# Performance work log

Measured on AMD Instinct MI355X. Metric: run time of the kernel, lower is better.

## Reference

```python
import jax, jax.numpy as jnp
import numpy as np

N_NODES, D, B, NEG2, DRUG_NUM = 20000, 512, 2048, 64, 2000
H1, H2 = 128, 64


def setup_inputs() -> dict:
    ks = jax.random.split(jax.random.key(0), 10)
    embed = jax.random.normal(ks[0], (N_NODES, D), dtype=jnp.float32)
    h = jax.random.randint(ks[1], (B, 1), 0, DRUG_NUM)
    t = jax.random.randint(ks[2], (B, 1), 0, N_NODES)
    n_s = jax.random.randint(ks[3], (B, NEG2), 0, DRUG_NUM)  # all < drug_num -> chunk branch
    s1 = 1.0 / np.sqrt(2 * D)
    s2 = 1.0 / np.sqrt(H1)
    s3 = 1.0 / np.sqrt(H2)
    W1 = jax.random.uniform(ks[4], (2 * D, H1), minval=-s1, maxval=s1, dtype=jnp.float32)
    b1 = jax.random.uniform(ks[5], (H1,), minval=-s1, maxval=s1, dtype=jnp.float32)
    W2 = jax.random.uniform(ks[6], (H1, H2), minval=-s2, maxval=s2, dtype=jnp.float32)
    b2 = jax.random.uniform(ks[7], (H2,), minval=-s2, maxval=s2, dtype=jnp.float32)
    W3 = jax.random.uniform(ks[8], (H2, 1), minval=-s3, maxval=s3, dtype=jnp.float32)
    b3 = jax.random.uniform(ks[9], (1,), minval=-s3, maxval=s3, dtype=jnp.float32)
    return {"embed": embed, "W1": W1, "b1": b1, "W2": W2, "b2": b2, "W3": W3, "b3": b3,
            "h": h, "t": t, "n_s": n_s}


def _mlp(x, W1, b1, W2, b2, W3, b3):
    # [..., 2D] -> [...] score
    x = jax.nn.relu(x @ W1 + b1)
    x = jax.nn.relu(x @ W2 + b2)
    return (x @ W3 + b3)[..., 0]


def reference(embed, W1, b1, W2, b2, W3, b3, h, t, n_s):
    K = n_s.shape[1] // 2
    n_t, n_h = n_s[:, :K], n_s[:, K:]
    h_e = embed[h]          # [B, 1, D]
    t_e = embed[t]          # [B, T, D]
    T = t.shape[1]
    # positive pairs: [B, T]
    pos = _mlp(jnp.concatenate([jnp.tile(h_e, (1, T, 1)), t_e], axis=-1),
               W1, b1, W2, b2, W3, b3)
    # corrupted-tail negatives: [B, K]
    neg1 = _mlp(jnp.concatenate([jnp.tile(h_e, (1, K, 1)), embed[n_t]], axis=-1),
                W1, b1, W2, b2, W3, b3)
    # corrupted-head negatives: [B, T*K] (T=1 here)
    neg2 = _mlp(jnp.concatenate([embed[n_h], jnp.tile(t_e, (1, K, 1))], axis=-1),
                W1, b1, W2, b2, W3, b3)
    neg = jnp.concatenate([neg1, neg2], axis=1)  # [B, 2K]
    return pos, neg
```

## Files before the change

### kernel.cpp

```cpp
#include <hip/hip_runtime.h>

#define DIM    512
#define BATCH  2048
#define NDRUG  2000
#define H1     128
#define H2     64
#define NITEM  65
#define SLAB   774144
#define W2F_OFF (4 * SLAB)
#define W1F_OFF (W2F_OFF + 4096)
#define X1_OFF  (W1F_OFF + 65536)
#define X2_OFF  (X1_OFF + 512000)

typedef __attribute__((ext_vector_type(8))) short short8;
typedef __attribute__((ext_vector_type(4))) float floatx4;

__device__ inline unsigned short f2bf(float x) {
    union { float f; unsigned u; } v; v.f = x;
    unsigned r = v.u + 0x7fffu + ((v.u >> 16) & 1u);
    return (unsigned short)(r >> 16);
}

__device__ inline short8 cvt8(const float* __restrict__ src) {
    float4 a = *(const float4*)src, b = *(const float4*)(src + 4);
    short8 v;
    v[0] = (short)f2bf(a.x); v[1] = (short)f2bf(a.y);
    v[2] = (short)f2bf(a.z); v[3] = (short)f2bf(a.w);
    v[4] = (short)f2bf(b.x); v[5] = (short)f2bf(b.y);
    v[6] = (short)f2bf(b.z); v[7] = (short)f2bf(b.w);
    return v;
}

__global__ __launch_bounds__(256) void prep(
    const float* __restrict__ embed, const float* __restrict__ W1,
    const float* __restrict__ W2, const int* __restrict__ t,
    float* __restrict__ ws)
{
    const int blk = blockIdx.x, tid = threadIdx.x;
    if (blk < 125) {
        short8* X1 = (short8*)(ws + X1_OFF);
        #pragma unroll
        for (int i = 0; i < 4; ++i) {
            int u = blk * 1024 + i * 256 + tid;
            int row = u >> 6, c = u & 63;
            X1[u] = cvt8(embed + (size_t)row * DIM + c * 8);
        }
    } else if (blk < 253) {
        short8* X2 = (short8*)(ws + X2_OFF);
        #pragma unroll
        for (int i = 0; i < 4; ++i) {
            int u = (blk - 125) * 1024 + i * 256 + tid;
            int row = u >> 6, c = u & 63;
            X2[u] = cvt8(embed + (size_t)t[row] * DIM + c * 8);
        }
    } else if (blk < 255) {
        short8* W1f = (short8*)(ws + W1F_OFF);
        #pragma unroll
        for (int i = 0; i < 32; ++i) {
            int item = (blk - 253) * 8192 + i * 256 + tid;
            int frag = item >> 6, lane = item & 63;
            int half = frag >> 7, ktot = (frag >> 3) & 15, nt = frag & 7;
            int n = lane & 15, q = lane >> 4;
            short8 v;
            #pragma unroll
            for (int j = 0; j < 8; ++j) {
                int k = half * DIM + ktot * 32 + q * 8 + j;
                v[j] = (short)f2bf(W1[k * H1 + nt * 16 + n]);
            }
            W1f[item] = v;
        }
    } else {
        short8* W2f = (short8*)(ws + W2F_OFF);
        #pragma unroll
        for (int i = 0; i < 4; ++i) {
            int item = i * 256 + tid;
            int frag = item >> 6, lane = item & 63;
            int kt = frag >> 2, nt = frag & 3;
            int n = lane & 15, q = lane >> 4;
            short8 v;
            #pragma unroll
            for (int j = 0; j < 8; ++j)
                v[j] = (short)f2bf(W2[(kt * 32 + q * 8 + j) * H2 + nt * 16 + n]);
            W2f[item] = v;
        }
    }
}

__global__ __launch_bounds__(256) void layer1_mfma(float* __restrict__ ws)
{
    const short8* W1f = (const short8*)(ws + W1F_OFF);
    const int lane = threadIdx.x & 63;
    const int w    = blockIdx.x * 4 + (threadIdx.x >> 6);
    const int n = lane & 15, q = lane >> 4;

    const short8* Xrow;
    float* obase;
    int half, ntsel, kc;
    if (w < 2000) {
        int rt = w >> 4, rem = w & 15, cg = rem >> 2;
        kc = rem & 3;
        Xrow = (const short8*)(ws + X1_OFF) + (size_t)(rt * 16 + n) * 64 + kc * 16;
        half  = cg >> 1;
        ntsel = (cg & 1) * 4;
        obase = ws + (size_t)kc * SLAB + half * (NDRUG * H1)
                   + (size_t)(rt * 16) * H1 + (cg & 1) * 64;
    } else {
        int w2 = w - 2000;
        int rt = w2 >> 3, rem = w2 & 7, cg = rem >> 2;
        kc = rem & 3;
        Xrow = (const short8*)(ws + X2_OFF) + (size_t)(rt * 16 + n) * 64 + kc * 16;
        half  = 1;
        ntsel = cg * 4;
        obase = ws + (size_t)kc * SLAB + 2 * (NDRUG * H1)
                   + (size_t)(rt * 16) * H1 + cg * 64;
    }

    floatx4 acc[4];
    #pragma unroll
    for (int nt = 0; nt < 4; ++nt) acc[nt] = (floatx4){0.f, 0.f, 0.f, 0.f};

    #pragma unroll
    for (int kt = 0; kt < 4; ++kt) {
        short8 af = Xrow[kt * 4 + q];
        #pragma unroll
        for (int nt = 0; nt < 4; ++nt) {
            short8 bf = W1f[(size_t)((half * 16 + kc * 4 + kt) * 8 + ntsel + nt) * 64 + lane];
            acc[nt] = __builtin_amdgcn_mfma_f32_16x16x32_bf16(af, bf, acc[nt], 0, 0, 0);
        }
    }

    #pragma unroll
    for (int nt = 0; nt < 4; ++nt)
        #pragma unroll
        for (int reg = 0; reg < 4; ++reg)
            obase[(q * 4 + reg) * H1 + nt * 16 + n] = acc[nt][reg];
}

__global__ __launch_bounds__(256) void reduce4(float* __restrict__ ws)
{
    int i = (blockIdx.x * 256 + threadIdx.x) * 8;
    #pragma unroll
    for (int half = 0; half < 2; ++half) {
        int o = i + half * 4;
        float4 a = *(const float4*)(ws + o);
        float4 b = *(const float4*)(ws + SLAB + o);
        float4 c = *(const float4*)(ws + 2 * SLAB + o);
        float4 d = *(const float4*)(ws + 3 * SLAB + o);
        a.x += b.x + c.x + d.x;  a.y += b.y + c.y + d.y;
        a.z += b.z + c.z + d.z;  a.w += b.w + c.w + d.w;
        *(float4*)(ws + o) = a;
    }
}

__global__ __launch_bounds__(256) void score_mfma(
    const float* __restrict__ ws,
    const float* __restrict__ b1, const float* __restrict__ b2,
    const float* __restrict__ W3, const float* __restrict__ b3,
    const int* __restrict__ h, const int* __restrict__ ns,
    float* __restrict__ out)
{
    const float* P  = ws;
    const float* Q  = ws + NDRUG * H1;
    const float* Qt = Q + NDRUG * H1;
    const short8* W2f = (const short8*)(ws + W2F_OFF);

    const int lane = threadIdx.x & 63;
    const int wv   = threadIdx.x >> 6;
    const int tile = blockIdx.x * 4 + wv;
    const int n = lane & 15, q = lane >> 4;

    const int sg   = tile * 16 + n;
    const int b    = sg / NITEM;
    const int item = sg - b * NITEM;
    const float *Pr, *Qr;
    if (item == 0)       { Pr = P + h[b] * H1;                        Qr = Qt + b * H1; }
    else if (item <= 32) { Pr = P + h[b] * H1;                        Qr = Q + ns[b * 64 + item - 1] * H1; }
    else                 { Pr = P + ns[b * 64 + 32 + item - 33] * H1; Qr = Qt + b * H1; }

    floatx4 acc[4];
    #pragma unroll
    for (int nt = 0; nt < 4; ++nt) acc[nt] = (floatx4){0.f, 0.f, 0.f, 0.f};

    #pragma unroll
    for (int kt = 0; kt < 4; ++kt) {
        const int kb = kt * 32 + q * 8;
        float4 p0 = *(const float4*)(Pr + kb);
        float4 p1 = *(const float4*)(Pr + kb + 4);
        float4 q0 = *(const float4*)(Qr + kb);
        float4 q1 = *(const float4*)(Qr + kb + 4);
        float4 c0 = *(const float4*)(b1 + kb);
        float4 c1 = *(const float4*)(b1 + kb + 4);
        short8 af;
        af[0] = (short)f2bf(fmaxf(p0.x + q0.x + c0.x, 0.f));
        af[1] = (short)f2bf(fmaxf(p0.y + q0.y + c0.y, 0.f));
        af[2] = (short)f2bf(fmaxf(p0.z + q0.z + c0.z, 0.f));
        af[3] = (short)f2bf(fmaxf(p0.w + q0.w + c0.w, 0.f));
        af[4] = (short)f2bf(fmaxf(p1.x + q1.x + c1.x, 0.f));
        af[5] = (short)f2bf(fmaxf(p1.y + q1.y + c1.y, 0.f));
        af[6] = (short)f2bf(fmaxf(p1.z + q1.z + c1.z, 0.f));
        af[7] = (short)f2bf(fmaxf(p1.w + q1.w + c1.w, 0.f));
        #pragma unroll
        for (int nt = 0; nt < 4; ++nt) {
            short8 bf = W2f[(kt * 4 + nt) * 64 + lane];
            acc[nt] = __builtin_amdgcn_mfma_f32_16x16x32_bf16(af, bf, acc[nt], 0, 0, 0);
        }
    }

    float part[4];
    #pragma unroll
    for (int reg = 0; reg < 4; ++reg) {
        float sum = 0.f;
        #pragma unroll
        for (int nt = 0; nt < 4; ++nt) {
            int j = nt * 16 + n;
            sum = fmaf(fmaxf(acc[nt][reg] + b2[j], 0.f), W3[j], sum);
        }
        part[reg] = sum;
    }
    #pragma unroll
    for (int m = 1; m < 16; m <<= 1) {
        #pragma unroll
        for (int reg = 0; reg < 4; ++reg)
            part[reg] += __shfl_xor(part[reg], m, 64);
    }
    if (n == 0) {
        const float base3 = b3[0];
        #pragma unroll
        for (int reg = 0; reg < 4; ++reg) {
            int gid = tile * 16 + q * 4 + reg;
            int bb  = gid / NITEM;
            int it  = gid - bb * NITEM;
            float val = part[reg] + base3;
            if (it == 0) out[bb] = val;
            else         out[BATCH + bb * 64 + (it - 1)] = val;
        }
    }
}

extern "C" void kernel_launch(void* const* d_in, const int* in_sizes, int n_in,
                              void* d_out, int out_size, void* d_ws, size_t ws_size,
                              hipStream_t stream) {
    const float* embed = (const float*)d_in[0];
    const float* W1    = (const float*)d_in[1];
    const float* b1    = (const float*)d_in[2];
    const float* W2    = (const float*)d_in[3];
    const float* b2    = (const float*)d_in[4];
    const float* W3    = (const float*)d_in[5];
    const float* b3    = (const float*)d_in[6];
    const int*   h     = (const int*)d_in[7];
    const int*   t     = (const int*)d_in[8];
    const int*   ns    = (const int*)d_in[9];
    float* out = (float*)d_out;
    float* ws  = (float*)d_ws;

    prep<<<256, 256, 0, stream>>>(embed, W1, W2, t, ws);
    layer1_mfma<<<756, 256, 0, stream>>>(ws);
    reduce4<<<SLAB / (256 * 8), 256, 0, stream>>>(ws);
    score_mfma<<<(BATCH * NITEM) / 64, 256, 0, stream>>>(ws, b1, b2, W3, b3,
                                                         h, ns, out);
}
```

Before: 127.2 us.

## Drop split-K partial slabs and reduce kernel; fold b1 into layer1 output

Layer 1 now has each wave compute one 16-column tile over the full K range with two interleaved accumulators, instead of splitting K four ways into separate slabs. This removes the reduce4 kernel launch and the round trip of four partial slabs through memory. The b1 bias is added once to the tail half inside layer1 rather than per score item, and the W1 fragment prep is spread across 64 blocks instead of 2. The bf16 packing is also rewritten to build 32-bit pairs. In exchange, each layer1 wave runs a longer serial MFMA chain, leaving less parallelism per output tile.

```diff
diff --git a/kernel.cpp b/kernel.cpp
--- a/kernel.cpp
+++ b/kernel.cpp
@@ -7,28 +7,30 @@
 #define H2     64
 #define NITEM  65
 #define SLAB   774144
-#define W2F_OFF (4 * SLAB)
-#define W1F_OFF (W2F_OFF + 4096)
-#define X1_OFF  (W1F_OFF + 65536)
-#define X2_OFF  (X1_OFF + 512000)
+#define W2F_OFF  (SLAB)
+#define W1F_OFF  (W2F_OFF + 4096)
+#define X1_OFF   (W1F_OFF + 65536)
+#define X2_OFF   (X1_OFF + 512000)
 
 typedef __attribute__((ext_vector_type(8))) short short8;
 typedef __attribute__((ext_vector_type(4))) float floatx4;
 
-__device__ inline unsigned short f2bf(float x) {
+__device__ inline unsigned f2bf(float x) {
     union { float f; unsigned u; } v; v.f = x;
     unsigned r = v.u + 0x7fffu + ((v.u >> 16) & 1u);
-    return (unsigned short)(r >> 16);
+    return r >> 16;
+}
+
+__device__ inline unsigned pkbf(float a, float b) {
+    return f2bf(a) | (f2bf(b) << 16);
 }
 
 __device__ inline short8 cvt8(const float* __restrict__ src) {
     float4 a = *(const float4*)src, b = *(const float4*)(src + 4);
-    short8 v;
-    v[0] = (short)f2bf(a.x); v[1] = (short)f2bf(a.y);
-    v[2] = (short)f2bf(a.z); v[3] = (short)f2bf(a.w);
-    v[4] = (short)f2bf(b.x); v[5] = (short)f2bf(b.y);
-    v[6] = (short)f2bf(b.z); v[7] = (short)f2bf(b.w);
-    return v;
+    union { short8 s; unsigned u[4]; } v;
+    v.u[0] = pkbf(a.x, a.y); v.u[1] = pkbf(a.z, a.w);
+    v.u[2] = pkbf(b.x, b.y); v.u[3] = pkbf(b.z, b.w);
+    return v.s;
 }
 
 __global__ __launch_bounds__(256) void prep(
@@ -53,22 +55,19 @@
             int row = u >> 6, c = u & 63;
             X2[u] = cvt8(embed + (size_t)t[row] * DIM + c * 8);
         }
-    } else if (blk < 255) {
+    } else if (blk < 317) {
         short8* W1f = (short8*)(ws + W1F_OFF);
-        #pragma unroll
-        for (int i = 0; i < 32; ++i) {
-            int item = (blk - 253) * 8192 + i * 256 + tid;
-            int frag = item >> 6, lane = item & 63;
-            int half = frag >> 7, ktot = (frag >> 3) & 15, nt = frag & 7;
-            int n = lane & 15, q = lane >> 4;
-            short8 v;
-            #pragma unroll
-            for (int j = 0; j < 8; ++j) {
-                int k = half * DIM + ktot * 32 + q * 8 + j;
-                v[j] = (short)f2bf(W1[k * H1 + nt * 16 + n]);
-            }
-            W1f[item] = v;
-        }
+        int item = (blk - 253) * 256 + tid;
+        int frag = item >> 6, lane = item & 63;
+        int half = frag >> 7, kt = (frag >> 3) & 15, nt = frag & 7;
+        int n = lane & 15, q = lane >> 4;
+        short8 v;
+        #pragma unroll
+        for (int j = 0; j < 8; ++j) {
+            int k = half * DIM + kt * 32 + q * 8 + j;
+            v[j] = (short)f2bf(W1[k * H1 + nt * 16 + n]);
+        }
+        W1f[item] = v;
     } else {
         short8* W2f = (short8*)(ws + W2F_OFF);
         #pragma unroll
@@ -86,7 +85,8 @@
     }
 }
 
-__global__ __launch_bounds__(256) void layer1_mfma(float* __restrict__ ws)
+__global__ __launch_bounds__(256) void layer1_mfma(
+    float* __restrict__ ws, const float* __restrict__ b1)
 {
     const short8* W1f = (const short8*)(ws + W1F_OFF);
     const int lane = threadIdx.x & 63;
@@ -95,67 +95,48 @@
 
     const short8* Xrow;
     float* obase;
-    int half, ntsel, kc;
+    int half, nt;
+    bool tail;
     if (w < 2000) {
-        int rt = w >> 4, rem = w & 15, cg = rem >> 2;
-        kc = rem & 3;
-        Xrow = (const short8*)(ws + X1_OFF) + (size_t)(rt * 16 + n) * 64 + kc * 16;
-        half  = cg >> 1;
-        ntsel = (cg & 1) * 4;
-        obase = ws + (size_t)kc * SLAB + half * (NDRUG * H1)
-                   + (size_t)(rt * 16) * H1 + (cg & 1) * 64;
+        int rt = w >> 4, cv = w & 15;
+        tail = cv >= 8;
+        nt   = cv & 7;
+        half = tail ? 1 : 0;
+        Xrow = (const short8*)(ws + X1_OFF) + (size_t)(rt * 16 + n) * 64;
+        obase = ws + (tail ? NDRUG * H1 : 0) + (size_t)(rt * 16) * H1 + nt * 16;
     } else {
         int w2 = w - 2000;
-        int rt = w2 >> 3, rem = w2 & 7, cg = rem >> 2;
-        kc = rem & 3;
-        Xrow = (const short8*)(ws + X2_OFF) + (size_t)(rt * 16 + n) * 64 + kc * 16;
-        half  = 1;
-        ntsel = cg * 4;
-        obase = ws + (size_t)kc * SLAB + 2 * (NDRUG * H1)
-                   + (size_t)(rt * 16) * H1 + cg * 64;
-    }
-
-    floatx4 acc[4];
-    #pragma unroll
-    for (int nt = 0; nt < 4; ++nt) acc[nt] = (floatx4){0.f, 0.f, 0.f, 0.f};
-
-    #pragma unroll
-    for (int kt = 0; kt < 4; ++kt) {
-        short8 af = Xrow[kt * 4 + q];
-        #pragma unroll
-        for (int nt = 0; nt < 4; ++nt) {
-            short8 bf = W1f[(size_t)((half * 16 + kc * 4 + kt) * 8 + ntsel + nt) * 64 + lane];
-            acc[nt] = __builtin_amdgcn_mfma_f32_16x16x32_bf16(af, bf, acc[nt], 0, 0, 0);
-        }
-    }
-
-    #pragma unroll
-    for (int nt = 0; nt < 4; ++nt)
-        #pragma unroll
-        for (int reg = 0; reg < 4; ++reg)
-            obase[(q * 4 + reg) * H1 + nt * 16 + n] = acc[nt][reg];
-}
-
-__global__ __launch_bounds__(256) void reduce4(float* __restrict__ ws)
-{
-    int i = (blockIdx.x * 256 + threadIdx.x) * 8;
-    #pragma unroll
-    for (int half = 0; half < 2; ++half) {
-        int o = i + half * 4;
-        float4 a = *(const float4*)(ws + o);
-        float4 b = *(const float4*)(ws + SLAB + o);
-        float4 c = *(const float4*)(ws + 2 * SLAB + o);
-        float4 d = *(const float4*)(ws + 3 * SLAB + o);
-        a.x += b.x + c.x + d.x;  a.y += b.y + c.y + d.y;
-        a.z += b.z + c.z + d.z;  a.w += b.w + c.w + d.w;
-        *(float4*)(ws + o) = a;
-    }
+        int rt = w2 >> 3;
+        nt   = w2 & 7;
+        half = 1;
+        tail = true;
+        Xrow = (const short8*)(ws + X2_OFF) + (size_t)(rt * 16 + n) * 64;
+        obase = ws + 2 * (NDRUG * H1) + (size_t)(rt * 16) * H1 + nt * 16;
+    }
+
+    floatx4 acc0 = (floatx4){0.f, 0.f, 0.f, 0.f};
+    floatx4 acc1 = (floatx4){0.f, 0.f, 0.f, 0.f};
+    const int fbase = (half * 16) * 8 + nt;
+    #pragma unroll
+    for (int kt = 0; kt < 16; kt += 2) {
+        short8 a0 = Xrow[kt * 4 + q];
+        short8 a1 = Xrow[(kt + 1) * 4 + q];
+        short8 b0 = W1f[(size_t)(fbase + kt * 8) * 64 + lane];
+        short8 b1f = W1f[(size_t)(fbase + (kt + 1) * 8) * 64 + lane];
+        acc0 = __builtin_amdgcn_mfma_f32_16x16x32_bf16(a0, b0, acc0, 0, 0, 0);
+        acc1 = __builtin_amdgcn_mfma_f32_16x16x32_bf16(a1, b1f, acc1, 0, 0, 0);
+    }
+
+    const float badd = tail ? b1[nt * 16 + n] : 0.f;
+    #pragma unroll
+    for (int reg = 0; reg < 4; ++reg)
+        obase[(q * 4 + reg) * H1 + n] = acc0[reg] + acc1[reg] + badd;
 }
 
 __global__ __launch_bounds__(256) void score_mfma(
     const float* __restrict__ ws,
-    const float* __restrict__ b1, const float* __restrict__ b2,
-    const float* __restrict__ W3, const float* __restrict__ b3,
+    const float* __restrict__ b2, const float* __restrict__ W3,
+    const float* __restrict__ b3,
     const int* __restrict__ h, const int* __restrict__ ns,
     float* __restrict__ out)
 {
@@ -188,21 +169,15 @@
         float4 p1 = *(const float4*)(Pr + kb + 4);
         float4 q0 = *(const float4*)(Qr + kb);
         float4 q1 = *(const float4*)(Qr + kb + 4);
-        float4 c0 = *(const float4*)(b1 + kb);
-        float4 c1 = *(const float4*)(b1 + kb + 4);
-        short8 af;
-        af[0] = (short)f2bf(fmaxf(p0.x + q0.x + c0.x, 0.f));
-        af[1] = (short)f2bf(fmaxf(p0.y + q0.y + c0.y, 0.f));
-        af[2] = (short)f2bf(fmaxf(p0.z + q0.z + c0.z, 0.f));
-        af[3] = (short)f2bf(fmaxf(p0.w + q0.w + c0.w, 0.f));
-        af[4] = (short)f2bf(fmaxf(p1.x + q1.x + c1.x, 0.f));
-        af[5] = (short)f2bf(fmaxf(p1.y + q1.y + c1.y, 0.f));
-        af[6] = (short)f2bf(fmaxf(p1.z + q1.z + c1.z, 0.f));
-        af[7] = (short)f2bf(fmaxf(p1.w + q1.w + c1.w, 0.f));
+        union { short8 s; unsigned u[4]; } A;
+        A.u[0] = pkbf(fmaxf(p0.x + q0.x, 0.f), fmaxf(p0.y + q0.y, 0.f));
+        A.u[1] = pkbf(fmaxf(p0.z + q0.z, 0.f), fmaxf(p0.w + q0.w, 0.f));
+        A.u[2] = pkbf(fmaxf(p1.x + q1.x, 0.f), fmaxf(p1.y + q1.y, 0.f));
+        A.u[3] = pkbf(fmaxf(p1.z + q1.z, 0.f), fmaxf(p1.w + q1.w, 0.f));
         #pragma unroll
         for (int nt = 0; nt < 4; ++nt) {
             short8 bf = W2f[(kt * 4 + nt) * 64 + lane];
-            acc[nt] = __builtin_amdgcn_mfma_f32_16x16x32_bf16(af, bf, acc[nt], 0, 0, 0);
+            acc[nt] = __builtin_amdgcn_mfma_f32_16x16x32_bf16(A.s, bf, acc[nt], 0, 0, 0);
         }
     }
 
@@ -253,9 +228,8 @@
     float* out = (float*)d_out;
     float* ws  = (float*)d_ws;
 
-    prep<<<256, 256, 0, stream>>>(embed, W1, W2, t, ws);
-    layer1_mfma<<<756, 256, 0, stream>>>(ws);
-    reduce4<<<SLAB / (256 * 8), 256, 0, stream>>>(ws);
-    score_mfma<<<(BATCH * NITEM) / 64, 256, 0, stream>>>(ws, b1, b2, W3, b3,
+    prep<<<318, 256, 0, stream>>>(embed, W1, W2, t, ws);
+    layer1_mfma<<<756, 256, 0, stream>>>(ws, b1);
+    score_mfma<<<(BATCH * NITEM) / 64, 256, 0, stream>>>(ws, b2, W3, b3,
                                                          h, ns, out);
 }
```

Measured after the change: 120.2 us. 5.5% less time.
